# Kernel tuning notes

Hardware: AMD Instinct MI355X
Metric: run time of the kernel (lower is better)

## Reference

```python
import jax, jax.numpy as jnp
import numpy as np

VOCAB, HID, LSTM_H, T_LEN, N_LAB, BATCH = 21128, 768, 128, 256, 9, 32


def _gru_dir(x, Wih, Whh, bih, bhh):
    # x: [B,T,D]; PyTorch GRU gate order: reset, update, new
    xp = jnp.einsum('btd,gd->tbg', x, Wih) + bih  # [T,B,3H]
    H = Whh.shape[1]
    def step(h, xt):
        gh = h @ Whh.T + bhh
        xr, xz, xn = jnp.split(xt, 3, axis=-1)
        hr, hz, hn = jnp.split(gh, 3, axis=-1)
        r = jax.nn.sigmoid(xr + hr)
        z = jax.nn.sigmoid(xz + hz)
        n = jnp.tanh(xn + r * hn)
        hnew = (1.0 - z) * n + z * h
        return hnew, hnew
    h0 = jnp.zeros((x.shape[0], H), x.dtype)
    _, hs = jax.lax.scan(step, h0, xp)
    return hs  # [T,B,H]


def _crf_llh(emissions, labels, trans, start, end):
    # emissions [B,T,L], labels [B,T]; full mask (all ones)
    e = jnp.transpose(emissions, (1, 0, 2))  # [T,B,L]
    emit_scores = jnp.take_along_axis(e, labels.T[:, :, None], axis=2)[:, :, 0]  # [T,B]
    trans_scores = trans[labels[:, :-1], labels[:, 1:]]  # [B,T-1]
    num = start[labels[:, 0]] + emit_scores.sum(0) + trans_scores.sum(1) + end[labels[:, -1]]
    def step(alpha, et):
        alpha = jax.nn.logsumexp(alpha[:, :, None] + trans[None] + et[:, None, :], axis=1)
        return alpha, None
    alpha0 = start + e[0]
    alpha, _ = jax.lax.scan(step, alpha0, e[1:])
    denom = jax.nn.logsumexp(alpha + end, axis=1)
    return num - denom  # [B]


def _viterbi(emissions, trans, start, end):
    e = jnp.transpose(emissions, (1, 0, 2))  # [T,B,L]
    def step(alpha, et):
        scores = alpha[:, :, None] + trans[None]  # [B,L_prev,L_cur]
        bp = jnp.argmax(scores, axis=1)
        alpha = jnp.max(scores, axis=1) + et
        return alpha, bp
    alpha0 = start + e[0]
    alpha, bps = jax.lax.scan(step, alpha0, e[1:])  # bps: [T-1,B,L]
    last = jnp.argmax(alpha + end, axis=1)  # [B]
    def back(y, bp):
        yprev = jnp.take_along_axis(bp, y[:, None], axis=1)[:, 0]
        return yprev, yprev
    _, path = jax.lax.scan(back, last, bps, reverse=True)  # [T-1,B]
    return jnp.concatenate([path, last[None]], axis=0).T  # [B,T]


def setup_inputs() -> dict:
    key = jax.random.key(0)
    ks = jax.random.split(key, 16)
    s = 0.02
    inp = {
        'input_ids': jax.random.randint(ks[0], (BATCH, T_LEN), 0, VOCAB),
        'attention_mask': jnp.ones((BATCH, T_LEN), jnp.int64 if jax.config.jax_enable_x64 else jnp.int32),
        'labels': jax.random.randint(ks[1], (BATCH, T_LEN), 0, N_LAB),
        'emb': jax.random.normal(ks[2], (VOCAB, HID), jnp.float32) * s,
        'Wih_f': jax.random.normal(ks[3], (3 * LSTM_H, HID), jnp.float32) * s,
        'Whh_f': jax.random.normal(ks[4], (3 * LSTM_H, LSTM_H), jnp.float32) * s,
        'bih_f': jnp.zeros((3 * LSTM_H,), jnp.float32),
        'bhh_f': jnp.zeros((3 * LSTM_H,), jnp.float32),
        'Wih_b': jax.random.normal(ks[5], (3 * LSTM_H, HID), jnp.float32) * s,
        'Whh_b': jax.random.normal(ks[6], (3 * LSTM_H, LSTM_H), jnp.float32) * s,
        'bih_b': jnp.zeros((3 * LSTM_H,), jnp.float32),
        'bhh_b': jnp.zeros((3 * LSTM_H,), jnp.float32),
        'Wlin': jax.random.normal(ks[7], (N_LAB, 2 * LSTM_H), jnp.float32) * s,
        'blin': jnp.zeros((N_LAB,), jnp.float32),
        'trans': jax.random.normal(ks[8], (N_LAB, N_LAB), jnp.float32) * 0.1,
        'start': jax.random.normal(ks[9], (N_LAB,), jnp.float32) * 0.1,
        'end': jax.random.normal(ks[10], (N_LAB,), jnp.float32) * 0.1,
    }
    return inp


def reference(input_ids, attention_mask, labels, emb, Wih_f, Whh_f, bih_f, bhh_f,
              Wih_b, Whh_b, bih_b, bhh_b, Wlin, blin, trans, start, end):
    x = emb[input_ids]  # [B,T,HID]
    hf = _gru_dir(x, Wih_f, Whh_f, bih_f, bhh_f)                 # [T,B,H]
    hb = _gru_dir(x[:, ::-1, :], Wih_b, Whh_b, bih_b, bhh_b)[::-1]  # [T,B,H]
    seq = jnp.concatenate([hf, hb], axis=-1).transpose(1, 0, 2)  # [B,T,2H]
    emissions = seq @ Wlin.T + blin                              # [B,T,L]
    decoded = _viterbi(emissions, trans, start, end)             # [B,T] int
    llh = _crf_llh(emissions, labels, trans, start, end)         # [B]
    loss = -jnp.mean(llh)
    return decoded, loss
```

## Files before the change

kernel.cpp:

```cpp
#include <hip/hip_runtime.h>
#include <math.h>

#define T_LEN 256
#define BATCH 32
#define HID   768
#define GH    384
#define LH    128
#define NLAB  9
#define M_TOT (T_LEN*BATCH)

typedef float v2f __attribute__((ext_vector_type(2)));
typedef _Float16 h8 __attribute__((ext_vector_type(8)));
typedef float f4 __attribute__((ext_vector_type(4)));

#define LO_SCALE 1024.f
#define LO_INV   (1.f/1024.f)

#define BC(x, i) __int_as_float(__builtin_amdgcn_ds_swizzle(__float_as_int(x), (i) << 5))

#define DPP_ADD(x, ctrl) \
  ((x) + __int_as_float(__builtin_amdgcn_update_dpp(0, __float_as_int(x), (ctrl), 0xF, 0xF, true)))

#define XOR4(x) __int_as_float(__builtin_amdgcn_ds_swizzle(__float_as_int(x), 0x101F))

#define BAR_LGKM() do {                                   \
    asm volatile("s_waitcnt lgkmcnt(0)" ::: "memory");    \
    __builtin_amdgcn_s_barrier();                         \
    asm volatile("" ::: "memory");                        \
  } while (0)

__global__ __launch_bounds__(256, 2) void k_gemm_xp(
    const int* __restrict__ ids, const float* __restrict__ emb,
    const float* __restrict__ Wf, const float* __restrict__ Wb,
    const float* __restrict__ bihf, const float* __restrict__ bihb,
    float* __restrict__ xp)
{
  __shared__ __align__(16) _Float16 Ah[128*40];
  __shared__ __align__(16) _Float16 Al[128*40];
  __shared__ __align__(16) _Float16 Bh[128*40];
  __shared__ __align__(16) _Float16 Bl[128*40];

  const int tid  = threadIdx.x;
  const int lane = tid & 63, w = tid >> 6;
  const int m0 = blockIdx.y * 128, n0 = blockIdx.x * 128;

  const int srow = tid >> 1, sk = (tid & 1) * 16;
  const int gm = m0 + srow;
  const int tok = ids[(gm & 31) * T_LEN + (gm >> 5)];
  const float* aG = emb + (size_t)tok * HID + sk;
  const int gn = n0 + srow;
  const float* bG = (gn < GH ? Wf + (size_t)gn * HID
                             : Wb + (size_t)(gn - GH) * HID) + sk;

  const int fr = lane & 15, fq = lane >> 4;
  const int mrow = (w & 1) * 64;
  const int ncol = (w >> 1) * 64;

  f4 acc[4][4];
  f4 acc2[4][4];
#pragma unroll
  for (int i = 0; i < 4; ++i)
#pragma unroll
    for (int j = 0; j < 4; ++j) { acc[i][j] = f4{0,0,0,0}; acc2[i][j] = f4{0,0,0,0}; }

  const int sb = srow * 40 + sk;

  float4 ra[4], rb[4];
#pragma unroll
  for (int c = 0; c < 4; ++c) {
    ra[c] = *reinterpret_cast<const float4*>(aG + 4 * c);
    rb[c] = *reinterpret_cast<const float4*>(bG + 4 * c);
  }

  for (int kt = 0; kt < HID / 32; ++kt) {
    __syncthreads();
#pragma unroll
    for (int m = 0; m < 2; ++m) {
      const float4* src = m ? rb : ra;
      _Float16* dsth = m ? Bh : Ah;
      _Float16* dstl = m ? Bl : Al;
#pragma unroll
      for (int seg = 0; seg < 2; ++seg) {
        float xs[8] = {src[2*seg].x, src[2*seg].y, src[2*seg].z, src[2*seg].w,
                       src[2*seg+1].x, src[2*seg+1].y, src[2*seg+1].z, src[2*seg+1].w};
        h8 hi, lo;
#pragma unroll
        for (int c = 0; c < 8; ++c) {
          _Float16 h = (_Float16)xs[c];
          hi[c] = h;
          lo[c] = (_Float16)((xs[c] - (float)h) * LO_SCALE);
        }
        *reinterpret_cast<h8*>(&dsth[sb + seg * 8]) = hi;
        *reinterpret_cast<h8*>(&dstl[sb + seg * 8]) = lo;
      }
    }
    if (kt + 1 < HID / 32) {
      const float* pa = aG + (kt + 1) * 32;
      const float* pb = bG + (kt + 1) * 32;
#pragma unroll
      for (int c = 0; c < 4; ++c) {
        ra[c] = *reinterpret_cast<const float4*>(pa + 4 * c);
        rb[c] = *reinterpret_cast<const float4*>(pb + 4 * c);
      }
    }
    __syncthreads();

    h8 fbh[4], fbl[4];
#pragma unroll
    for (int j = 0; j < 4; ++j) {
      const int off = (ncol + j * 16 + fr) * 40 + fq * 8;
      fbh[j] = *reinterpret_cast<const h8*>(&Bh[off]);
      fbl[j] = *reinterpret_cast<const h8*>(&Bl[off]);
    }
#pragma unroll
    for (int i = 0; i < 4; ++i) {
      const int off = (mrow + i * 16 + fr) * 40 + fq * 8;
      h8 fah = *reinterpret_cast<const h8*>(&Ah[off]);
      h8 fal = *reinterpret_cast<const h8*>(&Al[off]);
#pragma unroll
      for (int j = 0; j < 4; ++j) {
        acc[i][j]  = __builtin_amdgcn_mfma_f32_16x16x32_f16(fah, fbh[j], acc[i][j],  0, 0, 0);
        acc2[i][j] = __builtin_amdgcn_mfma_f32_16x16x32_f16(fah, fbl[j], acc2[i][j], 0, 0, 0);
        acc2[i][j] = __builtin_amdgcn_mfma_f32_16x16x32_f16(fal, fbh[j], acc2[i][j], 0, 0, 0);
      }
    }
  }

  float bcol[4];
#pragma unroll
  for (int j = 0; j < 4; ++j) {
    const int c = n0 + ncol + j * 16 + fr;
    bcol[j] = (c < GH) ? bihf[c] : bihb[c - GH];
  }
#pragma unroll
  for (int i = 0; i < 4; ++i)
#pragma unroll
    for (int j = 0; j < 4; ++j) {
      const int col = n0 + ncol + j * 16 + fr;
#pragma unroll
      for (int r = 0; r < 4; ++r) {
        const int row = m0 + mrow + i * 16 + fq * 4 + r;
        xp[(size_t)row * HID + col] = acc[i][j][r] + acc2[i][j][r] * LO_INV + bcol[j];
      }
    }
}

__global__ __attribute__((amdgpu_flat_work_group_size(1024, 1024),
                          amdgpu_waves_per_eu(4, 4)))
void k_gru(
    const float* __restrict__ xp,
    const float* __restrict__ Whhf, const float* __restrict__ Whhb,
    const float* __restrict__ bhhf, const float* __restrict__ bhhb,
    float* __restrict__ hbuf, float* __restrict__ lossp)
{
  __shared__ __align__(16) float hsp[2][144];
  const int tid = threadIdx.x;
  const int g   = tid >> 3;
  const int s   = tid & 7;
  const int bd  = blockIdx.x;
  const int dir = bd >> 5, b = bd & 31;
  const float* Whh = dir ? Whhb : Whhf;
  const float* bhh = dir ? bhhb : bhhf;

  if (bd == 0 && tid == 0) *lossp = 0.f;

  v2f w[3][8];
#pragma unroll
  for (int gate = 0; gate < 3; ++gate) {
    const float* wrow = Whh + (size_t)(gate * LH + g) * LH + s * 16;
#pragma unroll
    for (int j = 0; j < 4; ++j) {
      float4 w4 = *reinterpret_cast<const float4*>(wrow + j * 4);
      w[gate][2*j]   = v2f{w4.x, w4.y};
      w[gate][2*j+1] = v2f{w4.z, w4.w};
    }
  }
  const float br = bhh[g], bz = bhh[g + LH], bn = bhh[g + 2*LH];

  if (tid < LH) hsp[0][36*(tid >> 5) + (tid & 31)] = 0.f;

  const int t0   = dir ? (T_LEN - 1) : 0;
  const int dt   = dir ? -1 : 1;
  const float* xbase = xp + (size_t)b * HID + dir * GH + g;
  float* hob = hbuf + (size_t)b * 256 + dir * LH + g;

  float xr = 0.f, xz = 0.f, xn = 0.f;
  if (s == 0) {
    const float* p = xbase + (size_t)t0 * BATCH * HID;
    xr = p[0]; xz = p[LH]; xn = p[2*LH];
  }
  float hprev = 0.f;
  BAR_LGKM();

  const int rbase = 36 * (s >> 1) + 16 * (s & 1);

  int t = t0;
  for (int step = 0; step < T_LEN; ++step) {
    const int tn = (step < T_LEN - 1) ? (t + dt) : t;
    float xrn = 0.f, xzn = 0.f, xnn = 0.f;
    if (s == 0) {
      const float* p = xbase + (size_t)tn * BATCH * HID;
      xrn = p[0]; xzn = p[LH]; xnn = p[2*LH];
    }

    const float* hc = &hsp[step & 1][rbase];
    v2f ar0 = v2f{0.f,0.f}, ar1 = ar0, az0 = ar0, az1 = ar0, an0 = ar0, an1 = ar0;
#pragma unroll
    for (int j = 0; j < 4; ++j) {
      float4 h4 = *reinterpret_cast<const float4*>(hc + 4*j);
      v2f h0 = v2f{h4.x, h4.y}, h1 = v2f{h4.z, h4.w};
      ar0 = __builtin_elementwise_fma(w[0][2*j+0], h0, ar0);
      ar1 = __builtin_elementwise_fma(w[0][2*j+1], h1, ar1);
      az0 = __builtin_elementwise_fma(w[1][2*j+0], h0, az0);
      az1 = __builtin_elementwise_fma(w[1][2*j+1], h1, az1);
      an0 = __builtin_elementwise_fma(w[2][2*j+0], h0, an0);
      an1 = __builtin_elementwise_fma(w[2][2*j+1], h1, an1);
    }
    float ar = (ar0.x + ar0.y) + (ar1.x + ar1.y);
    float az = (az0.x + az0.y) + (az1.x + az1.y);
    float an = (an0.x + an0.y) + (an1.x + an1.y);
    ar = DPP_ADD(ar, 0xB1); ar = DPP_ADD(ar, 0x4E);
    az = DPP_ADD(az, 0xB1); az = DPP_ADD(az, 0x4E);
    an = DPP_ADD(an, 0xB1); an = DPP_ADD(an, 0x4E);
    {
      float art = XOR4(ar), azt = XOR4(az), ant = XOR4(an);
      ar += art; az += azt; an += ant;
    }

    if (s == 0) {
      float r  = __builtin_amdgcn_rcpf(1.f + __expf(-(xr + ar + br)));
      float z  = __builtin_amdgcn_rcpf(1.f + __expf(-(xz + az + bz)));
      float e2 = __expf(2.f * (xn + r * (an + bn)));
      float n  = (e2 - 1.f) * __builtin_amdgcn_rcpf(e2 + 1.f);
      float hnew = (1.f - z) * n + z * hprev;
      hprev = hnew;
      hsp[(step + 1) & 1][36*(g >> 5) + (g & 31)] = hnew;
      hob[(size_t)t * BATCH * 256] = hnew;
    }
    BAR_LGKM();
    xr = xrn; xz = xzn; xn = xnn;
    t = tn;
  }
}

__global__ __launch_bounds__(256, 1) void k_crf_fused(
    const float* __restrict__ hbuf, const float* __restrict__ Wlin,
    const float* __restrict__ blin, const int* __restrict__ labels,
    const float* __restrict__ trans, const float* __restrict__ start,
    const float* __restrict__ endv, float* __restrict__ dec_out,
    float* __restrict__ lossp)
{
  __shared__ float el[T_LEN * 10];
  __shared__ __align__(16) unsigned char bp8[(T_LEN - 1) * 16];
  const int b    = blockIdx.x;
  const int tid  = threadIdx.x;
  const int lane = tid & 63, w = tid >> 6;
  const int sub  = lane >> 4, l16 = lane & 15;

  float4 wreg[NLAB][4];
#pragma unroll
  for (int j = 0; j < NLAB; ++j)
#pragma unroll
    for (int c = 0; c < 4; ++c)
      wreg[j][c] = *reinterpret_cast<const float4*>(Wlin + j * 256 + l16 * 16 + c * 4);

  for (int k = 0; k < 16; ++k) {
    const int t = w * 64 + k * 4 + sub;
    const float* hp = hbuf + ((size_t)t * BATCH + b) * 256 + l16 * 16;
    const float4 h0 = *reinterpret_cast<const float4*>(hp);
    const float4 h1 = *reinterpret_cast<const float4*>(hp + 4);
    const float4 h2 = *reinterpret_cast<const float4*>(hp + 8);
    const float4 h3 = *reinterpret_cast<const float4*>(hp + 12);
    float acc[NLAB];
#pragma unroll
    for (int j = 0; j < NLAB; ++j) {
      const float4 w0 = wreg[j][0], w1 = wreg[j][1], w2 = wreg[j][2], w3 = wreg[j][3];
      float s0 = h0.x*w0.x + h0.y*w0.y + h0.z*w0.z + h0.w*w0.w;
      float s1 = h1.x*w1.x + h1.y*w1.y + h1.z*w1.z + h1.w*w1.w;
      float s2 = h2.x*w2.x + h2.y*w2.y + h2.z*w2.z + h2.w*w2.w;
      float s3 = h3.x*w3.x + h3.y*w3.y + h3.z*w3.z + h3.w*w3.w;
      acc[j] = (s0 + s1) + (s2 + s3);
    }
#pragma unroll
    for (int j = 0; j < NLAB; ++j) {
#pragma unroll
      for (int off = 1; off < 16; off <<= 1)
        acc[j] += __shfl_xor(acc[j], off);
    }
    if (l16 < NLAB) {
      float v = acc[0];
#pragma unroll
      for (int j = 1; j < NLAB; ++j) v = (l16 == j) ? acc[j] : v;
      el[t * 10 + l16] = v + blin[l16];
    }
  }
  __syncthreads();

  if (w == 0) {
    float tcol[NLAB];
#pragma unroll
    for (int i = 0; i < NLAB; ++i)
      tcol[i] = (lane < NLAB) ? trans[i * NLAB + lane] : 0.f;
    float alpha = (lane < NLAB) ? (start[lane] + el[lane]) : -3e38f;
    float et_next = (lane < NLAB) ? el[10 + lane] : 0.f;
    for (int s = 0; s < T_LEN - 1; ++s) {
      const float et = et_next;
      if (s < T_LEN - 2)
        et_next = (lane < NLAB) ? el[(s + 2) * 10 + lane] : 0.f;
      float v[NLAB];
      v[0] = BC(alpha, 0) + tcol[0];
      v[1] = BC(alpha, 1) + tcol[1];
      v[2] = BC(alpha, 2) + tcol[2];
      v[3] = BC(alpha, 3) + tcol[3];
      v[4] = BC(alpha, 4) + tcol[4];
      v[5] = BC(alpha, 5) + tcol[5];
      v[6] = BC(alpha, 6) + tcol[6];
      v[7] = BC(alpha, 7) + tcol[7];
      v[8] = BC(alpha, 8) + tcol[8];
      float v01 = (v[0] >= v[1]) ? v[0] : v[1];  int i01 = (v[0] >= v[1]) ? 0 : 1;
      float v23 = (v[2] >= v[3]) ? v[2] : v[3];  int i23 = (v[2] >= v[3]) ? 2 : 3;
      float v45 = (v[4] >= v[5]) ? v[4] : v[5];  int i45 = (v[4] >= v[5]) ? 4 : 5;
      float v67 = (v[6] >= v[7]) ? v[6] : v[7];  int i67 = (v[6] >= v[7]) ? 6 : 7;
      float va = (v01 >= v23) ? v01 : v23;       int ia = (v01 >= v23) ? i01 : i23;
      float vb = (v45 >= v67) ? v45 : v67;       int ib = (v45 >= v67) ? i45 : i67;
      float vc = (va >= vb) ? va : vb;           int ic = (va >= vb) ? ia : ib;
      float best = (vc >= v[8]) ? vc : v[8];     int bi = (vc >= v[8]) ? ic : 8;
      alpha = best + et;
      if (lane < NLAB) bp8[s * 16 + lane] = (unsigned char)bi;
    }
    float fin = alpha + ((lane < NLAB) ? endv[lane] : 0.f);
    float fv[NLAB];
    fv[0] = BC(fin, 0); fv[1] = BC(fin, 1); fv[2] = BC(fin, 2);
    fv[3] = BC(fin, 3); fv[4] = BC(fin, 4); fv[5] = BC(fin, 5);
    fv[6] = BC(fin, 6); fv[7] = BC(fin, 7); fv[8] = BC(fin, 8);
    float f01 = (fv[0] >= fv[1]) ? fv[0] : fv[1];  int j01 = (fv[0] >= fv[1]) ? 0 : 1;
    float f23 = (fv[2] >= fv[3]) ? fv[2] : fv[3];  int j23 = (fv[2] >= fv[3]) ? 2 : 3;
    float f45 = (fv[4] >= fv[5]) ? fv[4] : fv[5];  int j45 = (fv[4] >= fv[5]) ? 4 : 5;
    float f67 = (fv[6] >= fv[7]) ? fv[6] : fv[7];  int j67 = (fv[6] >= fv[7]) ? 6 : 7;
    float fa = (f01 >= f23) ? f01 : f23;           int ja = (f01 >= f23) ? j01 : j23;
    float fb = (f45 >= f67) ? f45 : f67;           int jb = (f45 >= f67) ? j45 : j67;
    float fc = (fa >= fb) ? fa : fb;               int jc = (fa >= fb) ? ja : jb;
    int last = (fc >= fv[8]) ? jc : 8;
    if (lane == 0) {
      int y = last;
      dec_out[b * T_LEN + (T_LEN - 1)] = (float)y;
      uint4 row = *reinterpret_cast<const uint4*>(&bp8[(T_LEN - 2) * 16]);
      for (int s = T_LEN - 2; s >= 0; --s) {
        uint4 nrow = row;
        if (s > 0) nrow = *reinterpret_cast<const uint4*>(&bp8[(s - 1) * 16]);
        unsigned wsel = (y < 4) ? row.x : ((y < 8) ? row.y : row.z);
        y = (int)((wsel >> ((y & 3) * 8)) & 0xffu);
        dec_out[b * T_LEN + s] = (float)y;
        row = nrow;
      }
    }
  } else if (w == 1) {
    float tcol[NLAB];
#pragma unroll
    for (int i = 0; i < NLAB; ++i)
      tcol[i] = (lane < NLAB) ? trans[i * NLAB + lane] : 0.f;
    float ca = (lane < NLAB) ? (start[lane] + el[lane]) : -3e38f;
    float et_next = (lane < NLAB) ? el[10 + lane] : 0.f;
    for (int s = 0; s < T_LEN - 1; ++s) {
      const float et = et_next;
      if (s < T_LEN - 2)
        et_next = (lane < NLAB) ? el[(s + 2) * 10 + lane] : 0.f;
      float c[NLAB];
      c[0] = BC(ca, 0) + tcol[0];
      c[1] = BC(ca, 1) + tcol[1];
      c[2] = BC(ca, 2) + tcol[2];
      c[3] = BC(ca, 3) + tcol[3];
      c[4] = BC(ca, 4) + tcol[4];
      c[5] = BC(ca, 5) + tcol[5];
      c[6] = BC(ca, 6) + tcol[6];
      c[7] = BC(ca, 7) + tcol[7];
      c[8] = BC(ca, 8) + tcol[8];
      float m01 = fmaxf(c[0], c[1]), m23 = fmaxf(c[2], c[3]);
      float m45 = fmaxf(c[4], c[5]), m67 = fmaxf(c[6], c[7]);
      float m = fmaxf(fmaxf(fmaxf(m01, m23), fmaxf(m45, m67)), c[8]);
      float p0 = __expf(c[0]-m) + __expf(c[1]-m), p1 = __expf(c[2]-m) + __expf(c[3]-m);
      float p2 = __expf(c[4]-m) + __expf(c[5]-m), p3 = __expf(c[6]-m) + __expf(c[7]-m);
      float p = ((p0 + p1) + (p2 + p3)) + __expf(c[8]-m);
      ca = m + __logf(p) + et;
    }
    float fv[NLAB];
    fv[0] = BC(ca, 0) + endv[0];
    fv[1] = BC(ca, 1) + endv[1];
    fv[2] = BC(ca, 2) + endv[2];
    fv[3] = BC(ca, 3) + endv[3];
    fv[4] = BC(ca, 4) + endv[4];
    fv[5] = BC(ca, 5) + endv[5];
    fv[6] = BC(ca, 6) + endv[6];
    fv[7] = BC(ca, 7) + endv[7];
    fv[8] = BC(ca, 8) + endv[8];
    float mx = -3e38f;
#pragma unroll
    for (int j = 0; j < NLAB; ++j) mx = fmaxf(mx, fv[j]);
    float ps = 0.f;
#pragma unroll
    for (int j = 0; j < NLAB; ++j) ps += __expf(fv[j] - mx);
    float denom = mx + __logf(ps);

    const int* lb = labels + b * T_LEN;
    float part = 0.f;
    for (int t4 = 0; t4 < 4; ++t4) {
      int t = lane * 4 + t4;
      int l = lb[t];
      part += el[t * 10 + l];
      if (t > 0) part += trans[lb[t - 1] * NLAB + l];
    }
#pragma unroll
    for (int off = 32; off > 0; off >>= 1) part += __shfl_xor(part, off);
    if (lane == 0) {
      float num = part + start[lb[0]] + endv[lb[T_LEN - 1]];
      float llh = num - denom;
      atomicAdd(lossp, -llh * (1.0f / BATCH));
    }
  }
}

extern "C" void kernel_launch(void* const* d_in, const int* in_sizes, int n_in,
                              void* d_out, int out_size, void* d_ws, size_t ws_size,
                              hipStream_t stream) {
  const int*   ids    = (const int*)d_in[0];
  const int*   labels = (const int*)d_in[2];
  const float* emb    = (const float*)d_in[3];
  const float* Wihf   = (const float*)d_in[4];
  const float* Whhf   = (const float*)d_in[5];
  const float* bihf   = (const float*)d_in[6];
  const float* bhhf   = (const float*)d_in[7];
  const float* Wihb   = (const float*)d_in[8];
  const float* Whhb   = (const float*)d_in[9];
  const float* bihb   = (const float*)d_in[10];
  const float* bhhb   = (const float*)d_in[11];
  const float* Wlin   = (const float*)d_in[12];
  const float* blin   = (const float*)d_in[13];
  const float* trans  = (const float*)d_in[14];
  const float* start  = (const float*)d_in[15];
  const float* endv   = (const float*)d_in[16];

  float* xp    = (float*)d_ws;
  float* hbuf  = xp + (size_t)M_TOT * HID;
  float* out   = (float*)d_out;
  float* lossp = out + M_TOT;

  k_gemm_xp<<<dim3(6, 64), 256, 0, stream>>>(ids, emb, Wihf, Wihb, bihf, bihb, xp);
  k_gru<<<64, 1024, 0, stream>>>(xp, Whhf, Whhb, bhhf, bhhb, hbuf, lossp);
  k_crf_fused<<<BATCH, 256, 0, stream>>>(hbuf, Wlin, blin, labels, trans,
                                         start, endv, out, lossp);
}
```

Before: 425.6 us.

## Run GRU recurrence on MFMA with split-fp16 weights, batching 16 sequences per block

Replaces the per-sequence scalar FMA GRU recurrence (64 blocks of 1024 threads, one batch element each) with MFMA 16x16x32 fp16 matmuls. Each block handles 16 batch elements of one direction, and weights and hidden state are split into hi/lo fp16 pairs to keep near-fp32 accuracy. This cuts the per-step instruction count and DPP/swizzle reductions. In exchange, only 4 blocks run, and each step needs 9 MFMAs per kt in a serial dependency chain, so per-step latency now depends on MFMA latency.

```diff
diff --git a/kernel.cpp b/kernel.cpp
--- a/kernel.cpp
+++ b/kernel.cpp
@@ -17,11 +17,6 @@
 #define LO_INV   (1.f/1024.f)
 
 #define BC(x, i) __int_as_float(__builtin_amdgcn_ds_swizzle(__float_as_int(x), (i) << 5))
-
-#define DPP_ADD(x, ctrl) \
-  ((x) + __int_as_float(__builtin_amdgcn_update_dpp(0, __float_as_int(x), (ctrl), 0xF, 0xF, true)))
-
-#define XOR4(x) __int_as_float(__builtin_amdgcn_ds_swizzle(__float_as_int(x), 0x101F))
 
 #define BAR_LGKM() do {                                   \
     asm volatile("s_waitcnt lgkmcnt(0)" ::: "memory");    \
@@ -145,101 +140,134 @@
     }
 }
 
-__global__ __attribute__((amdgpu_flat_work_group_size(1024, 1024),
-                          amdgpu_waves_per_eu(4, 4)))
+__global__ __attribute__((amdgpu_flat_work_group_size(512, 512),
+                          amdgpu_waves_per_eu(2, 2)))
 void k_gru(
     const float* __restrict__ xp,
     const float* __restrict__ Whhf, const float* __restrict__ Whhb,
     const float* __restrict__ bhhf, const float* __restrict__ bhhb,
     float* __restrict__ hbuf, float* __restrict__ lossp)
 {
-  __shared__ __align__(16) float hsp[2][144];
-  const int tid = threadIdx.x;
-  const int g   = tid >> 3;
-  const int s   = tid & 7;
-  const int bd  = blockIdx.x;
-  const int dir = bd >> 5, b = bd & 31;
-  const float* Whh = dir ? Whhb : Whhf;
-  const float* bhh = dir ? bhhb : bhhf;
+  __shared__ __align__(16) _Float16 Hhi[2][16 * 136];
+  __shared__ __align__(16) _Float16 Hlo[2][16 * 136];
+
+  const int tid  = threadIdx.x;
+  const int lane = tid & 63, w = tid >> 6;
+  const int fr = lane & 15, fq = lane >> 4;
+  const int bd = blockIdx.x;
+  const int dir = bd >> 1;
+  const int b0  = (bd & 1) * 16;
+  const float* __restrict__ Whh = dir ? Whhb : Whhf;
+  const float* __restrict__ bhh = dir ? bhhb : bhhf;
 
   if (bd == 0 && tid == 0) *lossp = 0.f;
 
-  v2f w[3][8];
-#pragma unroll
-  for (int gate = 0; gate < 3; ++gate) {
-    const float* wrow = Whh + (size_t)(gate * LH + g) * LH + s * 16;
-#pragma unroll
-    for (int j = 0; j < 4; ++j) {
-      float4 w4 = *reinterpret_cast<const float4*>(wrow + j * 4);
-      w[gate][2*j]   = v2f{w4.x, w4.y};
-      w[gate][2*j+1] = v2f{w4.z, w4.w};
-    }
-  }
-  const float br = bhh[g], bz = bhh[g + LH], bn = bhh[g + 2*LH];
-
-  if (tid < LH) hsp[0][36*(tid >> 5) + (tid & 31)] = 0.f;
-
-  const int t0   = dir ? (T_LEN - 1) : 0;
-  const int dt   = dir ? -1 : 1;
-  const float* xbase = xp + (size_t)b * HID + dir * GH + g;
-  float* hob = hbuf + (size_t)b * 256 + dir * LH + g;
-
-  float xr = 0.f, xz = 0.f, xn = 0.f;
-  if (s == 0) {
-    const float* p = xbase + (size_t)t0 * BATCH * HID;
-    xr = p[0]; xz = p[LH]; xn = p[2*LH];
-  }
-  float hprev = 0.f;
+  const int ucol = 16 * w + fr;
+
+  h8 wbh[3][4], wbl[3][4];
+#pragma unroll
+  for (int gate = 0; gate < 3; ++gate)
+#pragma unroll
+    for (int kt = 0; kt < 4; ++kt) {
+      const float* src = Whh + (size_t)(gate * LH + ucol) * LH + kt * 32 + fq * 8;
+      float4 s0 = *reinterpret_cast<const float4*>(src);
+      float4 s1 = *reinterpret_cast<const float4*>(src + 4);
+      float xs[8] = {s0.x, s0.y, s0.z, s0.w, s1.x, s1.y, s1.z, s1.w};
+      h8 hi, lo;
+#pragma unroll
+      for (int c = 0; c < 8; ++c) {
+        _Float16 h = (_Float16)xs[c];
+        hi[c] = h;
+        lo[c] = (_Float16)((xs[c] - (float)h) * LO_SCALE);
+      }
+      wbh[gate][kt] = hi;
+      wbl[gate][kt] = lo;
+    }
+  const float br = bhh[ucol], bz = bhh[ucol + LH], bn = bhh[ucol + 2 * LH];
+
+  {
+    const int row = tid >> 5, seg = tid & 31;
+    *reinterpret_cast<unsigned long long*>(&Hhi[0][row * 136 + seg * 4]) = 0ull;
+    *reinterpret_cast<unsigned long long*>(&Hlo[0][row * 136 + seg * 4]) = 0ull;
+  }
+
+  const int t0 = dir ? (T_LEN - 1) : 0;
+  const int dt = dir ? -1 : 1;
+  const float* xp0 = xp + dir * GH + ucol;
+  float* hb0 = hbuf + dir * LH + ucol;
+
+  float hprev[4] = {0.f, 0.f, 0.f, 0.f};
+
+  float xg[3][4];
+#pragma unroll
+  for (int gate = 0; gate < 3; ++gate)
+#pragma unroll
+    for (int r = 0; r < 4; ++r)
+      xg[gate][r] = xp0[((size_t)t0 * 32 + b0 + fq * 4 + r) * HID + gate * LH];
+
   BAR_LGKM();
 
-  const int rbase = 36 * (s >> 1) + 16 * (s & 1);
-
   int t = t0;
+  int p = 0;
   for (int step = 0; step < T_LEN; ++step) {
     const int tn = (step < T_LEN - 1) ? (t + dt) : t;
-    float xrn = 0.f, xzn = 0.f, xnn = 0.f;
-    if (s == 0) {
-      const float* p = xbase + (size_t)tn * BATCH * HID;
-      xrn = p[0]; xzn = p[LH]; xnn = p[2*LH];
-    }
-
-    const float* hc = &hsp[step & 1][rbase];
-    v2f ar0 = v2f{0.f,0.f}, ar1 = ar0, az0 = ar0, az1 = ar0, an0 = ar0, an1 = ar0;
-#pragma unroll
-    for (int j = 0; j < 4; ++j) {
-      float4 h4 = *reinterpret_cast<const float4*>(hc + 4*j);
-      v2f h0 = v2f{h4.x, h4.y}, h1 = v2f{h4.z, h4.w};
-      ar0 = __builtin_elementwise_fma(w[0][2*j+0], h0, ar0);
-      ar1 = __builtin_elementwise_fma(w[0][2*j+1], h1, ar1);
-      az0 = __builtin_elementwise_fma(w[1][2*j+0], h0, az0);
-      az1 = __builtin_elementwise_fma(w[1][2*j+1], h1, az1);
-      an0 = __builtin_elementwise_fma(w[2][2*j+0], h0, an0);
-      an1 = __builtin_elementwise_fma(w[2][2*j+1], h1, an1);
-    }
-    float ar = (ar0.x + ar0.y) + (ar1.x + ar1.y);
-    float az = (az0.x + az0.y) + (az1.x + az1.y);
-    float an = (an0.x + an0.y) + (an1.x + an1.y);
-    ar = DPP_ADD(ar, 0xB1); ar = DPP_ADD(ar, 0x4E);
-    az = DPP_ADD(az, 0xB1); az = DPP_ADD(az, 0x4E);
-    an = DPP_ADD(an, 0xB1); an = DPP_ADD(an, 0x4E);
-    {
-      float art = XOR4(ar), azt = XOR4(az), ant = XOR4(an);
-      ar += art; az += azt; an += ant;
-    }
-
-    if (s == 0) {
-      float r  = __builtin_amdgcn_rcpf(1.f + __expf(-(xr + ar + br)));
-      float z  = __builtin_amdgcn_rcpf(1.f + __expf(-(xz + az + bz)));
-      float e2 = __expf(2.f * (xn + r * (an + bn)));
-      float n  = (e2 - 1.f) * __builtin_amdgcn_rcpf(e2 + 1.f);
-      float hnew = (1.f - z) * n + z * hprev;
-      hprev = hnew;
-      hsp[(step + 1) & 1][36*(g >> 5) + (g & 31)] = hnew;
-      hob[(size_t)t * BATCH * 256] = hnew;
-    }
+
+    h8 ahi[4], alo[4];
+#pragma unroll
+    for (int kt = 0; kt < 4; ++kt) {
+      const int off = fr * 136 + kt * 32 + fq * 8;
+      ahi[kt] = *reinterpret_cast<const h8*>(&Hhi[p][off]);
+      alo[kt] = *reinterpret_cast<const h8*>(&Hlo[p][off]);
+    }
+
+    f4 aR = f4{0,0,0,0}, aZ = aR, aN = aR, aR2 = aR, aZ2 = aR, aN2 = aR;
+#pragma unroll
+    for (int kt = 0; kt < 4; ++kt) {
+      aR  = __builtin_amdgcn_mfma_f32_16x16x32_f16(ahi[kt], wbh[0][kt], aR,  0, 0, 0);
+      aZ  = __builtin_amdgcn_mfma_f32_16x16x32_f16(ahi[kt], wbh[1][kt], aZ,  0, 0, 0);
+      aN  = __builtin_amdgcn_mfma_f32_16x16x32_f16(ahi[kt], wbh[2][kt], aN,  0, 0, 0);
+      aR2 = __builtin_amdgcn_mfma_f32_16x16x32_f16(ahi[kt], wbl[0][kt], aR2, 0, 0, 0);
+      aR2 = __builtin_amdgcn_mfma_f32_16x16x32_f16(alo[kt], wbh[0][kt], aR2, 0, 0, 0);
+      aZ2 = __builtin_amdgcn_mfma_f32_16x16x32_f16(ahi[kt], wbl[1][kt], aZ2, 0, 0, 0);
+      aZ2 = __builtin_amdgcn_mfma_f32_16x16x32_f16(alo[kt], wbh[1][kt], aZ2, 0, 0, 0);
+      aN2 = __builtin_amdgcn_mfma_f32_16x16x32_f16(ahi[kt], wbl[2][kt], aN2, 0, 0, 0);
+      aN2 = __builtin_amdgcn_mfma_f32_16x16x32_f16(alo[kt], wbh[2][kt], aN2, 0, 0, 0);
+    }
+
+    float xgn[3][4];
+#pragma unroll
+    for (int gate = 0; gate < 3; ++gate)
+#pragma unroll
+      for (int r = 0; r < 4; ++r)
+        xgn[gate][r] = xp0[((size_t)tn * 32 + b0 + fq * 4 + r) * HID + gate * LH];
+
+#pragma unroll
+    for (int r = 0; r < 4; ++r) {
+      float hr = aR[r] + aR2[r] * LO_INV + br;
+      float hz = aZ[r] + aZ2[r] * LO_INV + bz;
+      float hn = aN[r] + aN2[r] * LO_INV + bn;
+      float rg = __builtin_amdgcn_rcpf(1.f + __expf(-(xg[0][r] + hr)));
+      float zg = __builtin_amdgcn_rcpf(1.f + __expf(-(xg[1][r] + hz)));
+      float e2 = __expf(2.f * (xg[2][r] + rg * hn));
+      float ng = (e2 - 1.f) * __builtin_amdgcn_rcpf(e2 + 1.f);
+      float hnew = (1.f - zg) * ng + zg * hprev[r];
+      hprev[r] = hnew;
+      _Float16 hh = (_Float16)hnew;
+      _Float16 hl = (_Float16)((hnew - (float)hh) * LO_SCALE);
+      const int row = fq * 4 + r;
+      Hhi[p ^ 1][row * 136 + ucol] = hh;
+      Hlo[p ^ 1][row * 136 + ucol] = hl;
+      hb0[((size_t)t * 32 + b0 + row) * 256] = hnew;
+    }
+
     BAR_LGKM();
-    xr = xrn; xz = xzn; xn = xnn;
+    p ^= 1;
     t = tn;
+#pragma unroll
+    for (int gate = 0; gate < 3; ++gate)
+#pragma unroll
+      for (int r = 0; r < 4; ++r)
+        xg[gate][r] = xgn[gate][r];
   }
 }
 
@@ -445,7 +473,7 @@
   float* lossp = out + M_TOT;
 
   k_gemm_xp<<<dim3(6, 64), 256, 0, stream>>>(ids, emb, Wihf, Wihb, bihf, bihb, xp);
-  k_gru<<<64, 1024, 0, stream>>>(xp, Whhf, Whhb, bhhf, bhhb, hbuf, lossp);
+  k_gru<<<4, 512, 0, stream>>>(xp, Whhf, Whhb, bhhf, bhhb, hbuf, lossp);
   k_crf_fused<<<BATCH, 256, 0, stream>>>(hbuf, Wlin, blin, labels, trans,
                                          start, endv, out, lossp);
 }
```

New measurement: 549.3 us. 1.29x slower.
